# Kernel tuning notes

Hardware: AMD Instinct MI355X
Metric: run time of the kernel (lower is better)

Reference implementation:

```python
import jax, jax.numpy as jnp
import numpy as np

TEMPERATURE = 5.0

def setup_inputs() -> dict:
    key = jax.random.key(0)
    k1, k2 = jax.random.split(key)
    B, D = 8192, 128
    features = jax.random.normal(k1, (B, D), dtype=jnp.float32)
    labels = jax.random.randint(k2, (B,), 0, 100, dtype=jnp.int64)
    return {"features": features, "labels": labels, "fac_label": 3}


def reference(features, labels, fac_label):
    # features: [B, D], labels: [B]
    B = features.shape[0]
    # positive-pair mask; note original's mask_scale row-copy loop is a no-op,
    # so mask_scale == mask, and mask_cross_feature == ones (fac_label unused in effect)
    mask = (labels[:, None] == labels[None, :]).astype(features.dtype)  # [B, B]

    sim = jnp.matmul(features, features.T) / TEMPERATURE  # [B, B]
    logits_max = jax.lax.stop_gradient(jnp.max(sim, axis=1, keepdims=True))
    logits = sim - logits_max

    # remove self-contrast (diagonal)
    logits_mask = 1.0 - jnp.eye(B, dtype=features.dtype)
    mask = mask * logits_mask

    exp_logits = jnp.exp(logits) * logits_mask
    log_prob = logits - jnp.log(1e-12 + exp_logits.sum(axis=1, keepdims=True))

    mean_log_prob_pos_mask = (mask * log_prob).sum(axis=1)  # [B]
    # vectorized form of the per-element reciprocal loop: 1/count where count>0 else 0
    cnt = mask.sum(axis=1)
    recip = jnp.where(cnt == 0, 0.0, 1.0 / jnp.where(cnt == 0, 1.0, cnt))

    loss = -(mean_log_prob_pos_mask * recip).mean()
    return loss
```

## Files before the change

kernel.cpp:

```cpp
#include <hip/hip_runtime.h>


#define BN 8192
#define DK 128
#define INV_T 0.2f
#define C1F 0.28853901f
#define C40F 27.7258872f

#define TILES  528
#define RIDERS 32
#define PSLOTS 32

#define NCLS 100
#define PB 128
#define PROWS (BN / PB)

#define OFF_FB    0
#define OFF_PART  (2 * 1024 * 1024)
#define OFF_GP    (OFF_PART + PSLOTS * BN * 4)
#define OFF_HISTP (OFF_GP + PB * NCLS * DK * 4)
#define OFF_G     (OFF_HISTP + PB * NCLS * 4)
#define OFF_HIST  (OFF_G + NCLS * DK * 4)
#define OFF_BSUM  (OFF_HIST + 512)
#define OFF_CTR   (OFF_BSUM + 256)

typedef __attribute__((ext_vector_type(8))) short bf16x8;
typedef __attribute__((ext_vector_type(4))) float f32x4;

__device__ __forceinline__ unsigned short f2bf(float f) {
    unsigned u = __builtin_bit_cast(unsigned, f);
    u += 0x7fffu + ((u >> 16) & 1u);
    return (unsigned short)(u >> 16);
}

__device__ __forceinline__ float fexp2(float x) {
#if __has_builtin(__builtin_amdgcn_exp2f)
    return __builtin_amdgcn_exp2f(x);
#else
    float r; asm("v_exp_f32 %0, %1" : "=v"(r) : "v"(x)); return r;
#endif
}

__device__ __forceinline__ void load_lds16(const void* g, void* l) {
    __builtin_amdgcn_global_load_lds(
        (const __attribute__((address_space(1))) unsigned int*)g,
        (__attribute__((address_space(3))) unsigned int*)l, 16, 0, 0);
}

__global__ __launch_bounds__(256) void prep_kernel(const float* __restrict__ F,
                                                   const int* __restrict__ labels,
                                                   unsigned short* __restrict__ Fb,
                                                   float* __restrict__ part,
                                                   float* __restrict__ Gp,
                                                   int* __restrict__ histp,
                                                   unsigned int* __restrict__ ctr) {
    const int t  = threadIdx.x;
    const int b  = blockIdx.x;
    const int r0 = b * PROWS;

    if (b == 0 && t == 0) *ctr = 0u;

    {
        float4* pz = (float4*)part + (size_t)b * (PSLOTS * BN / 4 / PB);
#pragma unroll
        for (int k = 0; k < PSLOTS * BN / 4 / PB / 256; ++k)
            pz[k * 256 + t] = make_float4(0.f, 0.f, 0.f, 0.f);
    }

    const float4* F4  = (const float4*)F + (size_t)b * (PROWS * DK / 4);
    ushort4*      Fb4 = (ushort4*)Fb + (size_t)b * (PROWS * DK / 4);
#pragma unroll
    for (int k = 0; k < PROWS * DK / 4 / 256; ++k) {
        float4 v = F4[k * 256 + t];
        ushort4 o;
        o.x = f2bf(v.x); o.y = f2bf(v.y); o.z = f2bf(v.z); o.w = f2bf(v.w);
        Fb4[k * 256 + t] = o;
    }

    __shared__ int   ll[PROWS];
    __shared__ int   lh[NCLS];
    __shared__ float gl[2][NCLS][DK];
    float4* gl4 = (float4*)gl;
    if (t < NCLS) lh[t] = 0;
    if (t < PROWS) ll[t] = labels[r0 + t];
#pragma unroll
    for (int k = 0; k < 2 * NCLS * DK / 4 / 256; ++k)
        gl4[k * 256 + t] = make_float4(0.f, 0.f, 0.f, 0.f);
    __syncthreads();

    if (t < PROWS) atomicAdd(&lh[ll[t]], 1);

    {
        const int half = t >> 7, col = t & 127;
        const int rb   = half * (PROWS / 2);
        for (int rr = 0; rr < PROWS / 2; ++rr) {
            const int lr = rb + rr;
            gl[half][ll[lr]][col] += F[(size_t)(r0 + lr) * DK + col];
        }
    }
    __syncthreads();

    if (t < NCLS) histp[b * NCLS + t] = lh[t];
    const float* gl0 = (const float*)gl;
#pragma unroll
    for (int k = 0; k < NCLS * DK / 256; ++k) {
        const int idx = k * 256 + t;
        Gp[(size_t)b * (NCLS * DK) + idx] = gl0[idx] + gl0[NCLS * DK + idx];
    }
}

template <bool DIAGT>
__device__ __forceinline__ void supcon_tile(const short* __restrict__ Fb,
                                            float* __restrict__ part,
                                            int bx, int cy, char* smem) {
    const int t    = threadIdx.x;
    const int wave = t >> 6, lane = t & 63;
    const int quad = lane >> 4, l16 = lane & 15;
    const int rowBase = bx * 256 + wave * 64;
    const int colBase = cy * 256;

    const char* Btile = (const char*)Fb + (size_t)colBase * 256;
    const int   gso   = (t & 15) * 256 + (t >> 6) * 64 + ((t >> 4) & 3) * 16;
    char*       ldsw  = smem + wave * 1024;

#pragma unroll
    for (int tt = 0; tt < 4; ++tt)
        load_lds16(Btile + tt * 4096 + gso, ldsw + tt * 4096);

    bf16x8 a[4][4];
#pragma unroll
    for (int rt = 0; rt < 4; ++rt)
#pragma unroll
        for (int kt = 0; kt < 4; ++kt)
            a[rt][kt] = *(const bf16x8*)(Fb + (size_t)(rowBase + rt * 16 + l16) * DK
                                            + kt * 32 + quad * 8);

    float Zs[4][4];
#pragma unroll
    for (int rt = 0; rt < 4; ++rt)
#pragma unroll
        for (int r = 0; r < 4; ++r) Zs[rt][r] = 0.f;
    float Zcol[16];
#pragma unroll
    for (int j = 0; j < 16; ++j) Zcol[j] = 0.f;

    const int roffb = quad * 256 + l16 * 16;

    __syncthreads();

#pragma unroll
    for (int g = 0; g < 4; ++g) {
        if (g < 3) {
            char* dsth = smem + ((g + 1) & 1) * 16384 + wave * 1024;
#pragma unroll
            for (int tt = 0; tt < 4; ++tt)
                load_lds16(Btile + (size_t)((g + 1) * 4 + tt) * 4096 + gso,
                           dsth + tt * 4096);
        }
        const char* srch = smem + (g & 1) * 16384;
#pragma unroll
        for (int tt = 0; tt < 4; ++tt) {
            const int jt = g * 4 + tt;
            bf16x8 bb[4];
#pragma unroll
            for (int kt = 0; kt < 4; ++kt)
                bb[kt] = *(const bf16x8*)(srch + tt * 4096 + kt * 1024 + roffb);
            float Zc = 0.f;
#pragma unroll
            for (int rt = 0; rt < 4; ++rt) {
                f32x4 acc = {0.f, 0.f, 0.f, 0.f};
#pragma unroll
                for (int kt = 0; kt < 4; ++kt)
                    acc = __builtin_amdgcn_mfma_f32_16x16x32_bf16(a[rt][kt], bb[kt],
                                                                  acc, 0, 0, 0);
#pragma unroll
                for (int r = 0; r < 4; ++r) {
                    float e = fexp2(fmaf(acc[r], C1F, -40.0f));
                    if (DIAGT) {
                        if (colBase + jt * 16 + l16 == rowBase + rt * 16 + quad * 4 + r)
                            e = 0.f;
                    }
                    Zs[rt][r] += e;
                    Zc += e;
                }
            }
            if (!DIAGT) {
                Zc += __shfl_xor(Zc, 16);
                Zc += __shfl_xor(Zc, 32);
                Zcol[jt] = Zc;
            }
        }
        if (g < 3) __syncthreads();
    }

#pragma unroll
    for (int rt = 0; rt < 4; ++rt)
#pragma unroll
        for (int r = 0; r < 4; ++r) {
            float zz = Zs[rt][r];
#pragma unroll
            for (int h = 1; h < 16; h <<= 1) zz += __shfl_xor(zz, h);
            if (l16 == 0)
                part[(size_t)cy * BN + rowBase + rt * 16 + quad * 4 + r] = zz;
        }

    if (!DIAGT) {
#pragma unroll
        for (int jt = 0; jt < 16; ++jt)
            if (quad == 0)
                atomicAdd(&part[(size_t)bx * BN + colBase + jt * 16 + l16], Zcol[jt]);
    }
}

__global__ __launch_bounds__(256) void supcon_main(const short* __restrict__ Fb,
                                                   float* __restrict__ part,
                                                   const float* __restrict__ Gp,
                                                   const int* __restrict__ histp,
                                                   float* __restrict__ G,
                                                   int* __restrict__ hist) {
    __shared__ alignas(16) char smem[32768];
    const int bid = blockIdx.x;
    if (bid >= TILES) {
        const int base = (bid - TILES) * 256 + threadIdx.x;
        for (int idx = base; idx < NCLS * DK + NCLS; idx += RIDERS * 256) {
            if (idx < NCLS * DK) {
                float s = 0.f;
#pragma unroll 8
                for (int p = 0; p < PB; ++p) s += Gp[(size_t)p * (NCLS * DK) + idx];
                G[idx] = s;
            } else {
                const int c = idx - NCLS * DK;
                int s = 0;
#pragma unroll 8
                for (int p = 0; p < PB; ++p) s += histp[p * NCLS + c];
                hist[c] = s;
            }
        }
        return;
    }
    int k = bid;
    int bx = (int)((sqrtf(8.0f * (float)k + 1.0f) - 1.0f) * 0.5f);
    while ((bx + 1) * (bx + 2) / 2 <= k) ++bx;
    while (bx * (bx + 1) / 2 > k) --bx;
    const int cy = k - bx * (bx + 1) / 2;
    if (cy == bx) supcon_tile<true >(Fb, part, bx, cy, smem);
    else          supcon_tile<false>(Fb, part, bx, cy, smem);
}

__global__ __launch_bounds__(256) void supcon_finalize(const float* __restrict__ F,
                                                       const int* __restrict__ labels,
                                                       const float* __restrict__ part,
                                                       const float* __restrict__ G,
                                                       const int* __restrict__ hist,
                                                       float* __restrict__ bsums,
                                                       unsigned int* __restrict__ ctr,
                                                       float* __restrict__ out) {
    const int t = threadIdx.x;
    const int i = blockIdx.x * 256 + t;

    float Zm = 0.f;
#pragma unroll 8
    for (int c = 0; c < PSLOTS; ++c) Zm += part[(size_t)c * BN + i];

    const int   lbl = labels[i];
    const float cnt = (float)(hist[lbl] - 1);

    const float4* fr = (const float4*)(F + (size_t)i * DK);
    const float4* gr = (const float4*)(G + lbl * DK);
    float dot = 0.f, nrm = 0.f;
#pragma unroll 8
    for (int k = 0; k < DK / 4; ++k) {
        const float4 av = fr[k], gv = gr[k];
        dot += av.x * gv.x + av.y * gv.y + av.z * gv.z + av.w * gv.w;
        nrm += av.x * av.x + av.y * av.y + av.z * av.z + av.w * av.w;
    }

    const float mt = nrm * INV_T;
    const float A  = (dot - nrm) * INV_T;
    float term = 0.f;
    if (cnt > 0.5f)
        term = (A - cnt * mt) / cnt - __logf(1e-12f + Zm * __expf(C40F - mt));

    float sum = term;
#pragma unroll
    for (int h = 1; h < 64; h <<= 1) sum += __shfl_xor(sum, h);
    __shared__ float ss[4];
    if ((t & 63) == 0) ss[t >> 6] = sum;
    __syncthreads();
    if (t == 0) {
        bsums[blockIdx.x] = ss[0] + ss[1] + ss[2] + ss[3];
        __threadfence();
        const unsigned old = atomicAdd(ctr, 1u);
        if (old == (BN / 256) - 1) {
            __threadfence();
            float tot = 0.f;
            const volatile float* vb = bsums;
            for (int c = 0; c < BN / 256; ++c) tot += vb[c];
            out[0] = -tot * (1.0f / BN);
        }
    }
}

extern "C" void kernel_launch(void* const* d_in, const int* in_sizes, int n_in,
                              void* d_out, int out_size, void* d_ws, size_t ws_size,
                              hipStream_t stream) {
    const float* F      = (const float*)d_in[0];
    const int*   labels = (const int*)d_in[1];
    float* out = (float*)d_out;
    char*  ws  = (char*)d_ws;

    unsigned short* Fb    = (unsigned short*)(ws + OFF_FB);
    float*          part  = (float*)(ws + OFF_PART);
    float*          Gp    = (float*)(ws + OFF_GP);
    int*            histp = (int*)(ws + OFF_HISTP);
    float*          G     = (float*)(ws + OFF_G);
    int*            hist  = (int*)(ws + OFF_HIST);
    float*          bsums = (float*)(ws + OFF_BSUM);
    unsigned int*   ctr   = (unsigned int*)(ws + OFF_CTR);

    prep_kernel<<<PB, 256, 0, stream>>>(F, labels, Fb, part, Gp, histp, ctr);
    supcon_main<<<TILES + RIDERS, 256, 0, stream>>>((const short*)Fb, part,
                                                    Gp, histp, G, hist);
    supcon_finalize<<<BN / 256, 256, 0, stream>>>(F, labels, part, G, hist,
                                                  bsums, ctr, out);
}
```

Baseline: 118.2 us.

## Halve row tile to 128 rows, double tile count, reduce class sums via atomics

The symmetric Gram-matrix tiling changes from 256x256 to 128x256 tiles, doubling the block count to 1056 so the GPU's compute units are better filled. Partial column sums go to a separate set of 32 slots, and the finalize pass picks slots based on the row block. The per-class feature sums and histogram are now accumulated with atomics in prep behind a new zeroing kernel, replacing the rider blocks that reduced per-block partials. The cost is an extra kernel launch, more atomic traffic, and each B tile loaded into LDS being reused by half as many rows.

```diff
diff --git a/kernel.cpp b/kernel.cpp
--- a/kernel.cpp
+++ b/kernel.cpp
@@ -7,9 +7,8 @@
 #define C1F 0.28853901f
 #define C40F 27.7258872f
 
-#define TILES  528
-#define RIDERS 32
-#define PSLOTS 32
+#define TILES 1056
+#define PSLOTS 64
 
 #define NCLS 100
 #define PB 128
@@ -17,9 +16,7 @@
 
 #define OFF_FB    0
 #define OFF_PART  (2 * 1024 * 1024)
-#define OFF_GP    (OFF_PART + PSLOTS * BN * 4)
-#define OFF_HISTP (OFF_GP + PB * NCLS * DK * 4)
-#define OFF_G     (OFF_HISTP + PB * NCLS * 4)
+#define OFF_G     (OFF_PART + PSLOTS * BN * 4)
 #define OFF_HIST  (OFF_G + NCLS * DK * 4)
 #define OFF_BSUM  (OFF_HIST + 512)
 #define OFF_CTR   (OFF_BSUM + 256)
@@ -47,18 +44,29 @@
         (__attribute__((address_space(3))) unsigned int*)l, 16, 0, 0);
 }
 
+__global__ __launch_bounds__(256) void zero_kernel(float* __restrict__ G,
+                                                   int* __restrict__ hist,
+                                                   unsigned int* __restrict__ ctr) {
+    const int t = threadIdx.x;
+    float4* g4 = (float4*)G;
+#pragma unroll
+    for (int k = 0; k < (NCLS * DK / 4 + 255) / 256; ++k) {
+        const int idx = k * 256 + t;
+        if (idx < NCLS * DK / 4) g4[idx] = make_float4(0.f, 0.f, 0.f, 0.f);
+    }
+    if (t < NCLS) hist[t] = 0;
+    if (t == 0) *ctr = 0u;
+}
+
 __global__ __launch_bounds__(256) void prep_kernel(const float* __restrict__ F,
                                                    const int* __restrict__ labels,
                                                    unsigned short* __restrict__ Fb,
                                                    float* __restrict__ part,
-                                                   float* __restrict__ Gp,
-                                                   int* __restrict__ histp,
-                                                   unsigned int* __restrict__ ctr) {
+                                                   float* __restrict__ G,
+                                                   int* __restrict__ hist) {
     const int t  = threadIdx.x;
     const int b  = blockIdx.x;
     const int r0 = b * PROWS;
-
-    if (b == 0 && t == 0) *ctr = 0u;
 
     {
         float4* pz = (float4*)part + (size_t)b * (PSLOTS * BN / 4 / PB);
@@ -100,12 +108,13 @@
     }
     __syncthreads();
 
-    if (t < NCLS) histp[b * NCLS + t] = lh[t];
+    if (t < NCLS && lh[t]) atomicAdd(&hist[t], lh[t]);
     const float* gl0 = (const float*)gl;
 #pragma unroll
     for (int k = 0; k < NCLS * DK / 256; ++k) {
         const int idx = k * 256 + t;
-        Gp[(size_t)b * (NCLS * DK) + idx] = gl0[idx] + gl0[NCLS * DK + idx];
+        const int c   = idx >> 7;
+        if (lh[c]) atomicAdd(&G[idx], gl0[idx] + gl0[NCLS * DK + idx]);
     }
 }
 
@@ -116,7 +125,7 @@
     const int t    = threadIdx.x;
     const int wave = t >> 6, lane = t & 63;
     const int quad = lane >> 4, l16 = lane & 15;
-    const int rowBase = bx * 256 + wave * 64;
+    const int rowBase = bx * 128 + wave * 32;
     const int colBase = cy * 256;
 
     const char* Btile = (const char*)Fb + (size_t)colBase * 256;
@@ -127,24 +136,23 @@
     for (int tt = 0; tt < 4; ++tt)
         load_lds16(Btile + tt * 4096 + gso, ldsw + tt * 4096);
 
-    bf16x8 a[4][4];
-#pragma unroll
-    for (int rt = 0; rt < 4; ++rt)
+    bf16x8 a[2][4];
+#pragma unroll
+    for (int rt = 0; rt < 2; ++rt)
 #pragma unroll
         for (int kt = 0; kt < 4; ++kt)
             a[rt][kt] = *(const bf16x8*)(Fb + (size_t)(rowBase + rt * 16 + l16) * DK
                                             + kt * 32 + quad * 8);
 
-    float Zs[4][4];
-#pragma unroll
-    for (int rt = 0; rt < 4; ++rt)
+    float Zs[2][4];
+#pragma unroll
+    for (int rt = 0; rt < 2; ++rt)
 #pragma unroll
         for (int r = 0; r < 4; ++r) Zs[rt][r] = 0.f;
-    float Zcol[16];
-#pragma unroll
-    for (int j = 0; j < 16; ++j) Zcol[j] = 0.f;
-
-    const int roffb = quad * 256 + l16 * 16;
+    float Zcol[4];
+
+    const int    roffb   = quad * 256 + l16 * 16;
+    float* const colpart = part + (size_t)(32 + (bx >> 1)) * BN + colBase;
 
     __syncthreads();
 
@@ -165,9 +173,9 @@
 #pragma unroll
             for (int kt = 0; kt < 4; ++kt)
                 bb[kt] = *(const bf16x8*)(srch + tt * 4096 + kt * 1024 + roffb);
-            float Zc = 0.f;
-#pragma unroll
-            for (int rt = 0; rt < 4; ++rt) {
+            float Zc0 = 0.f, Zc1 = 0.f;
+#pragma unroll
+            for (int rt = 0; rt < 2; ++rt) {
                 f32x4 acc = {0.f, 0.f, 0.f, 0.f};
 #pragma unroll
                 for (int kt = 0; kt < 4; ++kt)
@@ -181,20 +189,26 @@
                             e = 0.f;
                     }
                     Zs[rt][r] += e;
-                    Zc += e;
+                    if (!DIAGT) { if (rt == 0) Zc0 += e; else Zc1 += e; }
                 }
             }
             if (!DIAGT) {
+                float Zc = Zc0 + Zc1;
                 Zc += __shfl_xor(Zc, 16);
                 Zc += __shfl_xor(Zc, 32);
-                Zcol[jt] = Zc;
+                Zcol[tt] = Zc;
             }
         }
         if (g < 3) __syncthreads();
-    }
-
-#pragma unroll
-    for (int rt = 0; rt < 4; ++rt)
+        if (!DIAGT && quad == 0) {
+#pragma unroll
+            for (int tt = 0; tt < 4; ++tt)
+                atomicAdd(colpart + (g * 4 + tt) * 16 + l16, Zcol[tt]);
+        }
+    }
+
+#pragma unroll
+    for (int rt = 0; rt < 2; ++rt)
 #pragma unroll
         for (int r = 0; r < 4; ++r) {
             float zz = Zs[rt][r];
@@ -203,48 +217,20 @@
             if (l16 == 0)
                 part[(size_t)cy * BN + rowBase + rt * 16 + quad * 4 + r] = zz;
         }
-
-    if (!DIAGT) {
-#pragma unroll
-        for (int jt = 0; jt < 16; ++jt)
-            if (quad == 0)
-                atomicAdd(&part[(size_t)bx * BN + colBase + jt * 16 + l16], Zcol[jt]);
-    }
 }
 
 __global__ __launch_bounds__(256) void supcon_main(const short* __restrict__ Fb,
-                                                   float* __restrict__ part,
-                                                   const float* __restrict__ Gp,
-                                                   const int* __restrict__ histp,
-                                                   float* __restrict__ G,
-                                                   int* __restrict__ hist) {
+                                                   float* __restrict__ part) {
     __shared__ alignas(16) char smem[32768];
     const int bid = blockIdx.x;
-    if (bid >= TILES) {
-        const int base = (bid - TILES) * 256 + threadIdx.x;
-        for (int idx = base; idx < NCLS * DK + NCLS; idx += RIDERS * 256) {
-            if (idx < NCLS * DK) {
-                float s = 0.f;
-#pragma unroll 8
-                for (int p = 0; p < PB; ++p) s += Gp[(size_t)p * (NCLS * DK) + idx];
-                G[idx] = s;
-            } else {
-                const int c = idx - NCLS * DK;
-                int s = 0;
-#pragma unroll 8
-                for (int p = 0; p < PB; ++p) s += histp[p * NCLS + c];
-                hist[c] = s;
-            }
-        }
-        return;
-    }
-    int k = bid;
-    int bx = (int)((sqrtf(8.0f * (float)k + 1.0f) - 1.0f) * 0.5f);
-    while ((bx + 1) * (bx + 2) / 2 <= k) ++bx;
-    while (bx * (bx + 1) / 2 > k) --bx;
-    const int cy = k - bx * (bx + 1) / 2;
-    if (cy == bx) supcon_tile<true >(Fb, part, bx, cy, smem);
-    else          supcon_tile<false>(Fb, part, bx, cy, smem);
+    int k0 = (int)sqrtf((float)bid);
+    while ((k0 + 1) * (k0 + 1) <= bid) ++k0;
+    while (k0 * k0 > bid) --k0;
+    int bx, cy;
+    if (bid < k0 * k0 + k0) { bx = 2 * k0 - 1; cy = bid - k0 * k0; }
+    else                    { bx = 2 * k0;     cy = bid - k0 * k0 - k0; }
+    if (cy == (bx >> 1)) supcon_tile<true >(Fb, part, bx, cy, smem);
+    else                 supcon_tile<false>(Fb, part, bx, cy, smem);
 }
 
 __global__ __launch_bounds__(256) void supcon_finalize(const float* __restrict__ F,
@@ -255,12 +241,16 @@
                                                        float* __restrict__ bsums,
                                                        unsigned int* __restrict__ ctr,
                                                        float* __restrict__ out) {
-    const int t = threadIdx.x;
-    const int i = blockIdx.x * 256 + t;
+    const int t  = threadIdx.x;
+    const int i  = blockIdx.x * 256 + t;
+    const int c2 = blockIdx.x;
 
     float Zm = 0.f;
 #pragma unroll 8
-    for (int c = 0; c < PSLOTS; ++c) Zm += part[(size_t)c * BN + i];
+    for (int k = 0; k < 32; ++k) {
+        const int slot = (k <= c2) ? k : 32 + k;
+        Zm += part[(size_t)slot * BN + i];
+    }
 
     const int   lbl = labels[i];
     const float cnt = (float)(hist[lbl] - 1);
@@ -311,16 +301,14 @@
 
     unsigned short* Fb    = (unsigned short*)(ws + OFF_FB);
     float*          part  = (float*)(ws + OFF_PART);
-    float*          Gp    = (float*)(ws + OFF_GP);
-    int*            histp = (int*)(ws + OFF_HISTP);
     float*          G     = (float*)(ws + OFF_G);
     int*            hist  = (int*)(ws + OFF_HIST);
     float*          bsums = (float*)(ws + OFF_BSUM);
     unsigned int*   ctr   = (unsigned int*)(ws + OFF_CTR);
 
-    prep_kernel<<<PB, 256, 0, stream>>>(F, labels, Fb, part, Gp, histp, ctr);
-    supcon_main<<<TILES + RIDERS, 256, 0, stream>>>((const short*)Fb, part,
-                                                    Gp, histp, G, hist);
+    zero_kernel<<<1, 256, 0, stream>>>(G, hist, ctr);
+    prep_kernel<<<PB, 256, 0, stream>>>(F, labels, Fb, part, G, hist);
+    supcon_main<<<TILES, 256, 0, stream>>>((const short*)Fb, part);
     supcon_finalize<<<BN / 256, 256, 0, stream>>>(F, labels, part, G, hist,
                                                   bsums, ctr, out);
 }
```

Measured after the change: 121.2 us. 1.03x slower.
